# Performance work log

Measured on AMD Instinct MI355X. Metric: run time of the kernel, lower is better.

The kernel has to match this reference:

```python
import jax, jax.numpy as jnp
import numpy as np
import math

NUM_HEADS = 16
D_KV = 64
D_MODEL = 1024
NUM_BUCKETS = 32
MAX_DISTANCE = 128
SEQ = 2048
BATCH = 2


def _relative_position_bucket(relative_position):
    # bidirectional T5 bucketing
    num_buckets = NUM_BUCKETS // 2  # 16
    buckets = (relative_position > 0).astype(jnp.int32) * num_buckets
    rp = jnp.abs(relative_position)
    max_exact = num_buckets // 2  # 8
    is_small = rp < max_exact
    rp_safe = jnp.maximum(rp, 1)  # avoid log(0); masked by is_small anyway
    rp_large = max_exact + (
        jnp.log(rp_safe.astype(jnp.float32) / max_exact)
        / math.log(MAX_DISTANCE / max_exact)
        * (num_buckets - max_exact)
    ).astype(jnp.int32)
    rp_large = jnp.minimum(rp_large, num_buckets - 1)
    return buckets + jnp.where(is_small, rp, rp_large)


def _position_bias(rel_bias_table, q_len, k_len):
    ctx = jnp.arange(q_len)[:, None]
    mem = jnp.arange(k_len)[None, :]
    buckets = _relative_position_bucket(mem - ctx)  # (q,k)
    vals = rel_bias_table[buckets]  # (q,k,h)
    return jnp.transpose(vals, (2, 0, 1))[None]  # (1,h,q,k)


def setup_inputs() -> dict:
    key = jax.random.key(0)
    ks = jax.random.split(key, 6)
    s = 1.0 / math.sqrt(D_MODEL)
    return {
        "hidden_states": jax.random.normal(ks[0], (BATCH, SEQ, D_MODEL), jnp.float32),
        "Wq": jax.random.normal(ks[1], (D_MODEL, NUM_HEADS * D_KV), jnp.float32) * s,
        "Wk": jax.random.normal(ks[2], (D_MODEL, NUM_HEADS * D_KV), jnp.float32) * s,
        "Wv": jax.random.normal(ks[3], (D_MODEL, NUM_HEADS * D_KV), jnp.float32) * s,
        "Wo": jax.random.normal(ks[4], (NUM_HEADS * D_KV, D_MODEL), jnp.float32) * s,
        "rel_bias_table": jax.random.normal(ks[5], (NUM_BUCKETS, NUM_HEADS), jnp.float32),
    }


def reference(hidden_states, Wq, Wk, Wv, Wo, rel_bias_table):
    b, s, _ = hidden_states.shape
    q = (hidden_states @ Wq).reshape(b, s, NUM_HEADS, D_KV).transpose(0, 2, 1, 3)
    k = (hidden_states @ Wk).reshape(b, s, NUM_HEADS, D_KV).transpose(0, 2, 1, 3)
    v = (hidden_states @ Wv).reshape(b, s, NUM_HEADS, D_KV).transpose(0, 2, 1, 3)
    # T5: NO query scaling, additive relative-position bias
    scores = jnp.einsum("bhqd,bhkd->bhqk", q, k) + _position_bias(rel_bias_table, s, s)
    attn = jax.nn.softmax(scores, axis=-1)  # dropout is identity in eval
    out = jnp.einsum("bhqk,bhkd->bhqd", attn, v)
    out = out.transpose(0, 2, 1, 3).reshape(b, s, NUM_HEADS * D_KV)
    return out @ Wo
```

## Files before the change

kernel.cpp:

```cpp
#include <hip/hip_runtime.h>
#include <hip/hip_bf16.h>
#include <math.h>

#define NUM_HEADS 16
#define D_KV 64
#define D_MODEL 1024
#define SEQ 2048
#define BATCH 2
#define LOG2E 1.4426950408889634f

using bf16x8 = __attribute__((ext_vector_type(8))) short;
using bf16x4 = __attribute__((ext_vector_type(4))) short;
using f32x4  = __attribute__((ext_vector_type(4))) float;

__device__ inline unsigned short f2bf(float f) {
  union { float f; unsigned int i; } v; v.f = f;
  unsigned int u = v.i;
  return (unsigned short)((u + 0x7FFFu + ((u >> 16) & 1u)) >> 16);
}
__device__ inline unsigned short f2bf_fast(float f) {
  union { float f; unsigned int i; } v; v.f = f;
  return (unsigned short)((v.i + 0x8000u) >> 16);
}

#if __has_builtin(__builtin_amdgcn_exp2f)
#define EXP2(x) __builtin_amdgcn_exp2f(x)
#else
#define EXP2(x) __expf((x) * 0.6931471805599453f)
#endif

__device__ inline unsigned int pk_bf16(float a, float b) {
#if __has_builtin(__builtin_amdgcn_cvt_pk_bf16_f32)
  auto v = __builtin_amdgcn_cvt_pk_bf16_f32(a, b);
  unsigned int u; __builtin_memcpy(&u, &v, 4);
  return u;
#else
  return ((unsigned int)f2bf_fast(b) << 16) | f2bf_fast(a);
#endif
}

__device__ inline void gld_lds16(const unsigned short* g, unsigned short* l) {
  __builtin_amdgcn_global_load_lds(
      (const __attribute__((address_space(1))) unsigned int*)g,
      (__attribute__((address_space(3))) unsigned int*)l, 16, 0, 0);
}

__global__ __launch_bounds__(256) void prep_kernel(const float* __restrict__ X,
                                                   const float* __restrict__ W0,
                                                   const float* __restrict__ W1,
                                                   const float* __restrict__ W2,
                                                   const float* __restrict__ W3,
                                                   const float* __restrict__ tbl,
                                                   unsigned short* __restrict__ xbf,
                                                   unsigned short* __restrict__ wt,
                                                   float* __restrict__ biasF) {
  __shared__ __align__(16) unsigned short T[64][72];
  int bid = blockIdx.x;
  int t = threadIdx.x;
  if (bid < 2048) {
    int i = (bid * 256 + t) * 8;
    __align__(16) unsigned short tmp[8];
#pragma unroll
    for (int e = 0; e < 8; e++) tmp[e] = f2bf(X[i + e]);
    *(uint4*)&xbf[i] = *(uint4*)tmp;
  } else if (bid < 3072) {
    int rem = bid - 2048;
    int z = rem >> 8, tid = rem & 255;
    const float* in = (z == 0) ? W0 : (z == 1) ? W1 : (z == 2) ? W2 : W3;
    unsigned short* o = wt + (long)z * 1048576;
    int r0 = (tid & 15) * 64, c0 = (tid >> 4) * 64;
#pragma unroll
    for (int i = 0; i < 2; i++) {
      int c = t + 256 * i; int r = c >> 3, k8 = (c & 7) * 8;
      const float* src = &in[(long)(r0 + r) * 1024 + c0 + k8];
      __align__(16) unsigned short tmp[8];
#pragma unroll
      for (int e = 0; e < 8; e++) tmp[e] = f2bf(src[e]);
      *(uint4*)&T[r][k8] = *(uint4*)tmp;
    }
    __syncthreads();
#pragma unroll
    for (int i = 0; i < 2; i++) {
      int c = t + 256 * i; int r = c >> 3, k8 = (c & 7) * 8;
      __align__(16) unsigned short tmp[8];
#pragma unroll
      for (int e = 0; e < 8; e++) tmp[e] = T[k8 + e][r];
      *(uint4*)&o[(long)(c0 + r) * 1024 + r0 + k8] = *(uint4*)tmp;
    }
  } else {
#pragma unroll
    for (int ii = 0; ii < 16; ii++) {
      int idx = t + 256 * ii;
      if (idx >= 4095) break;
      int rel = idx - 2047;
      int bucket = (rel > 0) ? 16 : 0;
      int rp = rel < 0 ? -rel : rel;
      int add;
      if (rp < 8) add = rp;
      else {
        int rl = 8 + (int)(logf((float)rp * 0.125f) / logf(16.0f) * 8.0f);
        add = rl < 15 ? rl : 15;
      }
      bucket += add;
#pragma unroll
      for (int h = 0; h < 16; h++) biasF[h * 4096 + idx] = tbl[bucket * 16 + h] * LOG2E;
    }
  }
}

__global__ __launch_bounds__(256) void gemm_kernel(const unsigned short* __restrict__ X,
                                                   const unsigned short* __restrict__ Wt,
                                                   unsigned short* __restrict__ out_b,
                                                   unsigned short* __restrict__ out_vt) {
  __shared__ __align__(16) unsigned short SMEM[128 * 136];
  unsigned short* As = SMEM;
  unsigned short* Bs = SMEM + 128 * 32;
  const int K = 1024;
  int m0 = blockIdx.x * 128;
  int n0 = blockIdx.y * 128;
  const unsigned short* W = Wt + (long)blockIdx.z * 1048576;
  unsigned short* outq = out_b + (long)blockIdx.z * 4194304;
  float scale = (blockIdx.z == 0) ? LOG2E : 1.0f;
  int t = threadIdx.x;
  int w = t >> 6, l = t & 63;
  int wr = (w >> 1) * 64, wc = (w & 1) * 64;
  int lr = l & 15, lq = l >> 4;
  f32x4 acc[4][4];
#pragma unroll
  for (int i = 0; i < 4; i++)
#pragma unroll
    for (int j = 0; j < 4; j++) acc[i][j] = (f32x4){0.f, 0.f, 0.f, 0.f};

  for (int k0 = 0; k0 < K; k0 += 32) {
#pragma unroll
    for (int i = 0; i < 2; i++) {
      int c = t + 256 * i;
      int r = c >> 2, kc = (c & 3) * 8;
      gld_lds16(&X[(long)(m0 + r) * K + k0 + kc], &As[c * 8]);
      gld_lds16(&W[(long)(n0 + r) * K + k0 + kc], &Bs[c * 8]);
    }
    __syncthreads();
    bf16x8 a[4], b[4];
#pragma unroll
    for (int mi = 0; mi < 4; mi++) a[mi] = *(const bf16x8*)&As[(wr + mi * 16 + lr) * 32 + lq * 8];
#pragma unroll
    for (int ni = 0; ni < 4; ni++) b[ni] = *(const bf16x8*)&Bs[(wc + ni * 16 + lr) * 32 + lq * 8];
#pragma unroll
    for (int mi = 0; mi < 4; mi++)
#pragma unroll
      for (int ni = 0; ni < 4; ni++)
        acc[mi][ni] = __builtin_amdgcn_mfma_f32_16x16x32_bf16(a[mi], b[ni], acc[mi][ni], 0, 0, 0);
    __syncthreads();
  }

  if (blockIdx.z == 2) {
    unsigned short* Cs = SMEM;
#pragma unroll
    for (int mi = 0; mi < 4; mi++)
#pragma unroll
      for (int ni = 0; ni < 4; ni++) {
        int nl = wc + ni * 16 + lr;
        int ml = wr + mi * 16 + lq * 4;
        unsigned int s0 = pk_bf16(acc[mi][ni][0], acc[mi][ni][1]);
        unsigned int s1 = pk_bf16(acc[mi][ni][2], acc[mi][ni][3]);
        *(uint2*)&Cs[nl * 136 + ml] = (uint2){s0, s1};
      }
    __syncthreads();
    int b2 = m0 >> 11, sbase = m0 & 2047;
#pragma unroll
    for (int i = 0; i < 8; i++) {
      int c = t + 256 * i;
      int row = c >> 4, ch = c & 15;
      uint4 v = *(const uint4*)&Cs[row * 136 + ch * 8];
      int n = n0 + row, h = n >> 6, d = n & 63;
      *(uint4*)&out_vt[(((long)(b2 * 16 + h) * 64 + d) << 11) + sbase + ch * 8] = v;
    }
  } else {
    unsigned short* Cs = SMEM;
#pragma unroll
    for (int mi = 0; mi < 4; mi++)
#pragma unroll
      for (int ni = 0; ni < 4; ni++)
#pragma unroll
        for (int r = 0; r < 4; r++)
          Cs[(wr + mi * 16 + lq * 4 + r) * 136 + wc + ni * 16 + lr] = f2bf(acc[mi][ni][r] * scale);
    __syncthreads();
    int b2 = m0 >> 11, sbase = m0 & 2047;
#pragma unroll
    for (int i = 0; i < 8; i++) {
      int c = t + 256 * i;
      int row = c >> 4, ch = c & 15;
      uint4 v = *(const uint4*)&Cs[row * 136 + ch * 8];
      int n = n0 + ch * 8, h = n >> 6, d = n & 63;
      *(uint4*)&outq[((long)(b2 * 16 + h) * 2048 + sbase + row) * 64 + d] = v;
    }
  }
}

__global__ __launch_bounds__(256) void ogemm_kernel(const unsigned short* __restrict__ X,
                                                    const unsigned short* __restrict__ W,
                                                    float* __restrict__ out) {
  __shared__ __align__(16) unsigned char SMEM[64 * 68 * 4];
  unsigned short* As = (unsigned short*)SMEM;
  unsigned short* Bs = As + 4096;
  float* Csf = (float*)SMEM;
  const int K = 1024;
  int m0 = blockIdx.x * 64;
  int n0 = blockIdx.y * 64;
  int t = threadIdx.x;
  int w = t >> 6, l = t & 63;
  int wr = (w >> 1) * 32, wc = (w & 1) * 32;
  int lr = l & 15, lq = l >> 4;
  f32x4 acc[2][2];
#pragma unroll
  for (int i = 0; i < 2; i++)
#pragma unroll
    for (int j = 0; j < 2; j++) acc[i][j] = (f32x4){0.f, 0.f, 0.f, 0.f};

  for (int k0 = 0; k0 < K; k0 += 64) {
#pragma unroll
    for (int i = 0; i < 2; i++) {
      int c = t + 256 * i;
      int p = c >> 8, r = (c >> 2) & 63, kc = (c & 3) * 8;
      gld_lds16(&X[(long)(m0 + r) * K + k0 + p * 32 + kc], &As[c * 8]);
      gld_lds16(&W[(long)(n0 + r) * K + k0 + p * 32 + kc], &Bs[c * 8]);
    }
    __syncthreads();
    bf16x8 a[2][2], b[2][2];
#pragma unroll
    for (int ks = 0; ks < 2; ks++) {
#pragma unroll
      for (int mi = 0; mi < 2; mi++) a[mi][ks] = *(const bf16x8*)&As[ks * 2048 + (wr + mi * 16 + lr) * 32 + lq * 8];
#pragma unroll
      for (int ni = 0; ni < 2; ni++) b[ni][ks] = *(const bf16x8*)&Bs[ks * 2048 + (wc + ni * 16 + lr) * 32 + lq * 8];
    }
#pragma unroll
    for (int ks = 0; ks < 2; ks++)
#pragma unroll
      for (int mi = 0; mi < 2; mi++)
#pragma unroll
        for (int ni = 0; ni < 2; ni++)
          acc[mi][ni] = __builtin_amdgcn_mfma_f32_16x16x32_bf16(a[mi][ks], b[ni][ks], acc[mi][ni], 0, 0, 0);
    __syncthreads();
  }

#pragma unroll
  for (int mi = 0; mi < 2; mi++)
#pragma unroll
    for (int ni = 0; ni < 2; ni++)
#pragma unroll
      for (int r = 0; r < 4; r++)
        Csf[(wr + mi * 16 + lq * 4 + r) * 68 + wc + ni * 16 + lr] = acc[mi][ni][r];
  __syncthreads();
#pragma unroll
  for (int i = 0; i < 4; i++) {
    int c = t + 256 * i;
    int row = c >> 4, ch = c & 15;
    float4 v = *(const float4*)&Csf[row * 68 + ch * 4];
    *(float4*)&out[(long)(m0 + row) * 1024 + n0 + ch * 4] = v;
  }
}

__global__ __launch_bounds__(512) void attn_kernel(const unsigned short* __restrict__ Q,
                                                   const unsigned short* __restrict__ Km,
                                                   const unsigned short* __restrict__ Vt,
                                                   const float* __restrict__ biasF,
                                                   unsigned short* __restrict__ O) {
  __shared__ __align__(16) unsigned short KV[4][4608];
  __shared__ __align__(16) float biasRf[2][2176];
  __shared__ __align__(16) unsigned short Ps[8 * 1280];
  int q0 = blockIdx.x * 128;
  int bh = blockIdx.y;
  int b_ = bh >> 4, h = bh & 15;
  const unsigned short* Qb = Q  + (long)bh * SEQ * 64;
  const unsigned short* Kb = Km + (long)bh * SEQ * 64;
  const unsigned short* Vb = Vt + (long)bh * 64 * SEQ;
  const float* btabF = biasF + h * 4096;
  int t = threadIdx.x;
  int w = t >> 6, l = t & 63;
  int g = w >> 2, wg = w & 3;
  int lr = l & 15, lq = l >> 4;
  int qw = wg * 32;

  int gbase = 1920 - q0;
  for (int i = t; i < 2176; i += 512) {
    int g0 = gbase + i;     if (g0 > 4094) g0 = 4094;
    int g1 = gbase + i + 1; if (g1 > 4094) g1 = 4094;
    biasRf[0][i] = btabF[g0];
    biasRf[1][i] = btabF[g1];
  }

  bf16x8 aq[2][2];
#pragma unroll
  for (int qt = 0; qt < 2; qt++)
#pragma unroll
    for (int ks = 0; ks < 2; ks++)
      aq[qt][ks] = *(const bf16x8*)&Qb[(long)(q0 + qw + qt * 16 + lr) * 64 + ks * 32 + lq * 8];

  int rs = t >> 3, fs = (t & 7) * 8;

  uint4 kpa = *(const uint4*)&Kb[(long)rs * 64 + fs];
  uint4 kpb = *(const uint4*)&Kb[(long)(64 + rs) * 64 + fs];
  uint4 vpa = *(const uint4*)&Vb[(long)rs * SEQ + fs];
  uint4 vpb = *(const uint4*)&Vb[(long)rs * SEQ + 64 + fs];
  *(uint4*)&KV[0][rs * 72 + fs] = kpa;
  *(uint4*)&KV[1][rs * 72 + fs] = kpb;
  *(uint4*)&KV[2][rs * 72 + fs] = vpa;
  *(uint4*)&KV[3][rs * 72 + fs] = vpb;

  f32x4 accO[4][2];
  float rsum[2] = {0.f, 0.f};
#pragma unroll
  for (int qt = 0; qt < 2; qt++)
#pragma unroll
    for (int dt = 0; dt < 4; dt++) accO[dt][qt] = (f32x4){0.f, 0.f, 0.f, 0.f};

  int vb = 127 + lq * 4 - qw - lr;
  int bj2 = vb & 1;
  const float* brow = biasRf[bj2];
  int pbc = vb - bj2 - 16;
  unsigned short* Pw = Ps + w * 1280;

  for (int i = 0; i < 16; i++) {
    __syncthreads();
    int k0 = (2 * i + g) * 64;
    bool more = i < 15;

    float2 bbl[5][2];
    int pb = pbc + k0;
#pragma unroll
    for (int m = 0; m < 5; m++) {
      bbl[m][0] = *(const float2*)&brow[pb + 16 * m];
      bbl[m][1] = *(const float2*)&brow[pb + 16 * m + 2];
    }

    bf16x8 bk[4][2];
#pragma unroll
    for (int kt = 0; kt < 4; kt++)
#pragma unroll
      for (int ks = 0; ks < 2; ks++)
        bk[kt][ks] = *(const bf16x8*)&KV[g][(kt * 16 + lr) * 72 + ks * 32 + lq * 8];

    if (more) {
      const unsigned short* Kn = Kb + (long)(2 * i + 2) * 64 * 64;
      const unsigned short* Vn = Vb + (2 * i + 2) * 64;
      kpa = *(const uint4*)&Kn[(long)rs * 64 + fs];
      kpb = *(const uint4*)&Kn[(long)(64 + rs) * 64 + fs];
      vpa = *(const uint4*)&Vn[(long)rs * SEQ + fs];
      vpb = *(const uint4*)&Vn[(long)rs * SEQ + 64 + fs];
    }

    f32x4 sacc[4][2];
#pragma unroll
    for (int kt = 0; kt < 4; kt++)
#pragma unroll
      for (int qt = 0; qt < 2; qt++) sacc[kt][qt] = (f32x4){0.f, 0.f, 0.f, 0.f};
#pragma unroll
    for (int ks = 0; ks < 2; ks++)
#pragma unroll
      for (int kt = 0; kt < 4; kt++)
#pragma unroll
        for (int qt = 0; qt < 2; qt++)
          sacc[kt][qt] = __builtin_amdgcn_mfma_f32_16x16x32_bf16(bk[kt][ks], aq[qt][ks], sacc[kt][qt], 0, 0, 0);

#pragma unroll
    for (int ktp = 0; ktp < 2; ktp++) {
#pragma unroll
      for (int kth = 0; kth < 2; kth++) {
        int kt = ktp * 2 + kth;
#pragma unroll
        for (int qt = 0; qt < 2; qt++) {
          int blk = kt - qt + 1;
          float p0 = EXP2(sacc[kt][qt][0] + bbl[blk][0].x);
          float p1 = EXP2(sacc[kt][qt][1] + bbl[blk][0].y);
          float p2 = EXP2(sacc[kt][qt][2] + bbl[blk][1].x);
          float p3 = EXP2(sacc[kt][qt][3] + bbl[blk][1].y);
          rsum[qt] += (p0 + p1) + (p2 + p3);
          *(uint2*)&Pw[(qt * 16 + lr) * 40 + kth * 16 + lq * 4] =
              (uint2){ pk_bf16(p0, p1), pk_bf16(p2, p3) };
        }
      }
      bf16x8 va8[4];
#pragma unroll
      for (int dt = 0; dt < 4; dt++)
        va8[dt] = *(const bf16x8*)&KV[2 + g][(dt * 16 + lr) * 72 + ktp * 32 + lq * 8];
      bf16x8 pb8[2];
#pragma unroll
      for (int qt = 0; qt < 2; qt++)
        pb8[qt] = *(const bf16x8*)&Pw[(qt * 16 + lr) * 40 + lq * 8];
#pragma unroll
      for (int qt = 0; qt < 2; qt++)
#pragma unroll
        for (int dt = 0; dt < 4; dt++)
          accO[dt][qt] = __builtin_amdgcn_mfma_f32_16x16x32_bf16(va8[dt], pb8[qt], accO[dt][qt], 0, 0, 0);
    }

    __syncthreads();
    if (more) {
      *(uint4*)&KV[0][rs * 72 + fs] = kpa;
      *(uint4*)&KV[1][rs * 72 + fs] = kpb;
      *(uint4*)&KV[2][rs * 72 + fs] = vpa;
      *(uint4*)&KV[3][rs * 72 + fs] = vpb;
    }
  }

#pragma unroll
  for (int qt = 0; qt < 2; qt++) {
    rsum[qt] += __shfl_xor(rsum[qt], 16);
    rsum[qt] += __shfl_xor(rsum[qt], 32);
  }

  float* mrg = (float*)&KV[0][0];
  int slot = (wg * 64 + l) * 34;
  if (g == 1) {
    float2* mp = (float2*)&mrg[slot];
    int j = 0;
#pragma unroll
    for (int dt = 0; dt < 4; dt++)
#pragma unroll
      for (int qt = 0; qt < 2; qt++) {
        mp[j++] = (float2){accO[dt][qt][0], accO[dt][qt][1]};
        mp[j++] = (float2){accO[dt][qt][2], accO[dt][qt][3]};
      }
    mp[16] = (float2){rsum[0], rsum[1]};
  }
  __syncthreads();
  if (g == 0) {
    const float2* mp = (const float2*)&mrg[slot];
    int j = 0;
#pragma unroll
    for (int dt = 0; dt < 4; dt++)
#pragma unroll
      for (int qt = 0; qt < 2; qt++) {
        float2 a = mp[j++], b2 = mp[j++];
        accO[dt][qt][0] += a.x;  accO[dt][qt][1] += a.y;
        accO[dt][qt][2] += b2.x; accO[dt][qt][3] += b2.y;
      }
    float2 ls = mp[16];
    float rl0 = 1.0f / (rsum[0] + ls.x);
    float rl1 = 1.0f / (rsum[1] + ls.y);
#pragma unroll
    for (int qt = 0; qt < 2; qt++) {
      float rl = qt ? rl1 : rl0;
      int q = q0 + qw + qt * 16 + lr;
#pragma unroll
      for (int dt = 0; dt < 4; dt++) {
        unsigned int s0 = ((unsigned int)f2bf(accO[dt][qt][1] * rl) << 16) | f2bf(accO[dt][qt][0] * rl);
        unsigned int s1 = ((unsigned int)f2bf(accO[dt][qt][3] * rl) << 16) | f2bf(accO[dt][qt][2] * rl);
        *(uint2*)&O[((long)(b_ * SEQ + q)) * 1024 + h * 64 + dt * 16 + lq * 4] = (uint2){s0, s1};
      }
    }
  }
}

extern "C" void kernel_launch(void* const* d_in, const int* in_sizes, int n_in,
                              void* d_out, int out_size, void* d_ws, size_t ws_size,
                              hipStream_t stream) {
  const float* X   = (const float*)d_in[0];
  const float* Wq  = (const float*)d_in[1];
  const float* Wk  = (const float*)d_in[2];
  const float* Wv  = (const float*)d_in[3];
  const float* Wo  = (const float*)d_in[4];
  const float* tbl = (const float*)d_in[5];

  unsigned short* wt    = (unsigned short*)d_ws;
  unsigned short* xbf   = wt + 4 * 1048576;
  unsigned short* q_ws  = xbf + 4194304;
  unsigned short* k_ws  = q_ws + 4194304;
  unsigned short* vt_ws = k_ws + 4194304;
  float* biasF = (float*)(vt_ws + 4194304);
  unsigned short* o_ws  = xbf;

  prep_kernel<<<3073, 256, 0, stream>>>(X, Wq, Wk, Wv, Wo, tbl, xbf, wt, biasF);
  gemm_kernel<<<dim3(32, 8, 3), 256, 0, stream>>>(xbf, wt, q_ws, vt_ws);
  attn_kernel<<<dim3(16, 32), 512, 0, stream>>>(q_ws, k_ws, vt_ws, biasF, o_ws);
  ogemm_kernel<<<dim3(64, 16), 256, 0, stream>>>(o_ws, wt + 3 * 1048576, (float*)d_out);
}
```

Baseline: 210.6 us.

## Keep softmax probabilities in registers and use constant bias for far tiles

The probability tile is no longer written to shared memory and read back. Each lane packs its exp values straight into the MFMA B operand, and the V fragments are loaded as two 4-element halves so their K ordering matches the register layout of P. Tiles far from the diagonal now use a constant bias value (the first or last table entry) instead of loading bias from LDS. This removes a shared-memory round trip and its LDS footprint per iteration, at the cost of narrower V loads and a branch whose thresholds must exactly match the bucket saturation range.

```diff
diff --git a/kernel.cpp b/kernel.cpp
--- a/kernel.cpp
+++ b/kernel.cpp
@@ -268,7 +268,6 @@
                                                    unsigned short* __restrict__ O) {
   __shared__ __align__(16) unsigned short KV[4][4608];
   __shared__ __align__(16) float biasRf[2][2176];
-  __shared__ __align__(16) unsigned short Ps[8 * 1280];
   int q0 = blockIdx.x * 128;
   int bh = blockIdx.y;
   int b_ = bh >> 4, h = bh & 15;
@@ -282,6 +281,8 @@
   int lr = l & 15, lq = l >> 4;
   int qw = wg * 32;
 
+  float bL = btabF[0], bH = btabF[4094];
+
   int gbase = 1920 - q0;
   for (int i = t; i < 2176; i += 512) {
     int g0 = gbase + i;     if (g0 > 4094) g0 = 4094;
@@ -319,7 +320,6 @@
   int bj2 = vb & 1;
   const float* brow = biasRf[bj2];
   int pbc = vb - bj2 - 16;
-  unsigned short* Pw = Ps + w * 1280;
 
   for (int i = 0; i < 16; i++) {
     __syncthreads();
@@ -327,11 +327,19 @@
     bool more = i < 15;
 
     float2 bbl[5][2];
-    int pb = pbc + k0;
-#pragma unroll
-    for (int m = 0; m < 5; m++) {
-      bbl[m][0] = *(const float2*)&brow[pb + 16 * m];
-      bbl[m][1] = *(const float2*)&brow[pb + 16 * m + 2];
+    int dq = k0 - q0;
+    if (dq >= 218 || dq <= -154) {
+      float bc = (dq >= 218) ? bH : bL;
+      float2 bc2 = (float2){bc, bc};
+#pragma unroll
+      for (int m = 0; m < 5; m++) { bbl[m][0] = bc2; bbl[m][1] = bc2; }
+    } else {
+      int pb = pbc + k0;
+#pragma unroll
+      for (int m = 0; m < 5; m++) {
+        bbl[m][0] = *(const float2*)&brow[pb + 16 * m];
+        bbl[m][1] = *(const float2*)&brow[pb + 16 * m + 2];
+      }
     }
 
     bf16x8 bk[4][2];
@@ -365,34 +373,35 @@
 
 #pragma unroll
     for (int ktp = 0; ktp < 2; ktp++) {
-#pragma unroll
-      for (int kth = 0; kth < 2; kth++) {
-        int kt = ktp * 2 + kth;
-#pragma unroll
-        for (int qt = 0; qt < 2; qt++) {
+      bf16x8 va8[4];
+#pragma unroll
+      for (int dt = 0; dt < 4; dt++) {
+        const unsigned short* vp = &KV[2 + g][(dt * 16 + lr) * 72 + ktp * 32 + lq * 4];
+        bf16x4 vlo = *(const bf16x4*)vp;
+        bf16x4 vhi = *(const bf16x4*)(vp + 16);
+        va8[dt] = __builtin_shufflevector(vlo, vhi, 0, 1, 2, 3, 4, 5, 6, 7);
+      }
+#pragma unroll
+      for (int qt = 0; qt < 2; qt++) {
+        unsigned int u[4];
+#pragma unroll
+        for (int kth = 0; kth < 2; kth++) {
+          int kt = ktp * 2 + kth;
           int blk = kt - qt + 1;
           float p0 = EXP2(sacc[kt][qt][0] + bbl[blk][0].x);
           float p1 = EXP2(sacc[kt][qt][1] + bbl[blk][0].y);
           float p2 = EXP2(sacc[kt][qt][2] + bbl[blk][1].x);
           float p3 = EXP2(sacc[kt][qt][3] + bbl[blk][1].y);
           rsum[qt] += (p0 + p1) + (p2 + p3);
-          *(uint2*)&Pw[(qt * 16 + lr) * 40 + kth * 16 + lq * 4] =
-              (uint2){ pk_bf16(p0, p1), pk_bf16(p2, p3) };
+          u[kth * 2]     = pk_bf16(p0, p1);
+          u[kth * 2 + 1] = pk_bf16(p2, p3);
         }
-      }
-      bf16x8 va8[4];
-#pragma unroll
-      for (int dt = 0; dt < 4; dt++)
-        va8[dt] = *(const bf16x8*)&KV[2 + g][(dt * 16 + lr) * 72 + ktp * 32 + lq * 8];
-      bf16x8 pb8[2];
-#pragma unroll
-      for (int qt = 0; qt < 2; qt++)
-        pb8[qt] = *(const bf16x8*)&Pw[(qt * 16 + lr) * 40 + lq * 8];
-#pragma unroll
-      for (int qt = 0; qt < 2; qt++)
+        union { unsigned int uu[4]; bf16x8 v; } pbu;
+        pbu.uu[0] = u[0]; pbu.uu[1] = u[1]; pbu.uu[2] = u[2]; pbu.uu[3] = u[3];
 #pragma unroll
         for (int dt = 0; dt < 4; dt++)
-          accO[dt][qt] = __builtin_amdgcn_mfma_f32_16x16x32_bf16(va8[dt], pb8[qt], accO[dt][qt], 0, 0, 0);
+          accO[dt][qt] = __builtin_amdgcn_mfma_f32_16x16x32_bf16(va8[dt], pbu.v, accO[dt][qt], 0, 0, 0);
+      }
     }
 
     __syncthreads();
```

After: 205.8 us. -2.3%, faster.
